# Performance work log

Measured on AMD Instinct MI355X. Metric: run time of the kernel, lower is better.

## Reference

```python
import jax, jax.numpy as jnp
import numpy as np

N_HEADS = 8
D_K = 64
SCALE = D_K ** -0.5


def setup_inputs() -> dict:
    key = jax.random.key(0)
    ks = jax.random.split(key, 5)
    B, C, H, W = 4, 512, 32, 32
    x = jax.random.normal(ks[0], (B, C, H, W), dtype=jnp.float32)
    Wp = jax.random.normal(ks[1], (3 * N_HEADS * D_K, C), dtype=jnp.float32) * (C ** -0.5)
    bp = jax.random.normal(ks[2], (3 * N_HEADS * D_K,), dtype=jnp.float32) * 0.02
    Wo = jax.random.normal(ks[3], (C, N_HEADS * D_K), dtype=jnp.float32) * ((N_HEADS * D_K) ** -0.5)
    bo = jax.random.normal(ks[4], (C,), dtype=jnp.float32) * 0.02
    return {"x": x, "Wp": Wp, "bp": bp, "Wo": Wo, "bo": bo}


def reference(x, Wp, bp, Wo, bo):
    # x: [B, C, H, W]; NOTE: the torch module defines GroupNorm but never calls it.
    B, C, H, W = x.shape
    s = H * W
    xs = x.reshape(B, C, s).transpose(0, 2, 1)          # [B, s, C]
    qkv = (xs @ Wp.T + bp).reshape(B, s, N_HEADS, 3 * D_K)
    q, k, v = jnp.split(qkv, 3, axis=-1)                 # each [B, s, h, d]
    attn = jnp.einsum('bihd,bjhd->bijh', q, k) * SCALE   # [B, s, s, h]
    attn = jax.nn.softmax(attn, axis=2)                  # softmax over j (keys)
    res = jnp.einsum('bijh,bjhd->bihd', attn, v)         # [B, s, h, d]
    res = res.reshape(B, s, N_HEADS * D_K)
    out = res @ Wo.T + bo + xs                           # residual add
    return out.transpose(0, 2, 1).reshape(B, C, H, W)
```

## Files before the change

### kernel.cpp

```cpp
#include <hip/hip_runtime.h>
#include <hip/hip_bf16.h>

typedef unsigned short u16;
typedef __attribute__((ext_vector_type(8))) short frag_ab;
typedef __attribute__((ext_vector_type(4))) float f32x4;
typedef _Float16 f16;
typedef __attribute__((ext_vector_type(4))) _Float16 f16x4;

#define LOG2E 1.44269504088896f

__device__ __forceinline__ float fast_exp2(float x) {
    return __builtin_amdgcn_exp2f(x);
}

__device__ __forceinline__ void gload_lds16(const u16* g, u16* s) {
    __builtin_amdgcn_global_load_lds((const __attribute__((address_space(1))) void*)g,
                                     (__attribute__((address_space(3))) void*)s, 16, 0, 0);
}
__device__ __forceinline__ void gload_lds16h(const f16* g, f16* s) {
    __builtin_amdgcn_global_load_lds((const __attribute__((address_space(1))) void*)g,
                                     (__attribute__((address_space(3))) void*)s, 16, 0, 0);
}

__device__ __forceinline__ void gemm64x128_bt_mainloop(
    const u16* __restrict__ A, const u16* __restrict__ B,
    int m0, int n0, f32x4 acc[2][4], u16* lds)
{
    const int tid = threadIdx.x;
    const int lane = tid & 63, quad = lane >> 4, l16 = lane & 15;
    const int wr = ((tid >> 7) & 1) * 32;
    const int wc = ((tid >> 6) & 1) * 64;
    const int srow = tid >> 3;
    const int scol = (tid & 7) * 8;

    u16* Asb[2] = {lds, lds + 12288};
    u16* Bsb[2] = {lds + 4096, lds + 16384};

#define STAGE_128(bi, k0) do {                                                \
        u16* As_ = Asb[bi]; u16* Bs_ = Bsb[bi];                               \
        _Pragma("unroll")                                                     \
        for (int p = 0; p < 2; ++p) {                                         \
            const int r = srow + p * 32;                                      \
            gload_lds16(A + (size_t)(m0 + r) * 512 + (k0) + scol,             \
                        As_ + r * 64 + scol);                                 \
        }                                                                     \
        _Pragma("unroll")                                                     \
        for (int p = 0; p < 4; ++p) {                                         \
            const int r = srow + p * 32;                                      \
            gload_lds16(B + (size_t)(n0 + r) * 512 + (k0) + scol,             \
                        Bs_ + r * 64 + scol);                                 \
        }                                                                     \
    } while (0)

    STAGE_128(0, 0);
    __syncthreads();
    #pragma unroll
    for (int t = 0; t < 8; ++t) {
        const int cur = t & 1;
        if (t < 7) STAGE_128(cur ^ 1, (t + 1) * 64);
        u16* Asc = Asb[cur];
        u16* Bsc = Bsb[cur];
        #pragma unroll
        for (int ks = 0; ks < 2; ++ks) {
            frag_ab a[2], b[4];
            #pragma unroll
            for (int mt = 0; mt < 2; ++mt)
                a[mt] = *(const frag_ab*)(Asc + (wr + mt * 16 + l16) * 64 + ks * 32 + quad * 8);
            #pragma unroll
            for (int nt = 0; nt < 4; ++nt)
                b[nt] = *(const frag_ab*)(Bsc + (wc + nt * 16 + l16) * 64 + ks * 32 + quad * 8);
            #pragma unroll
            for (int mt = 0; mt < 2; ++mt)
                #pragma unroll
                for (int nt = 0; nt < 4; ++nt)
                    acc[mt][nt] = __builtin_amdgcn_mfma_f32_16x16x32_bf16(a[mt], b[nt], acc[mt][nt], 0, 0, 0);
        }
        if (t < 7) __syncthreads();
    }
#undef STAGE_128
}

__device__ __forceinline__ void gemm64x64_bt_mainloop(
    const u16* __restrict__ A, const u16* __restrict__ B,
    int m0, int n0, f32x4 acc[2][2], u16* lds)
{
    const int tid = threadIdx.x;
    const int lane = tid & 63, quad = lane >> 4, l16 = lane & 15;
    const int wr = ((tid >> 7) & 1) * 32;
    const int wc = ((tid >> 6) & 1) * 32;
    const int srow = tid >> 3;
    const int scol = (tid & 7) * 8;

    u16* Asb[2] = {lds, lds + 8192};
    u16* Bsb[2] = {lds + 4096, lds + 12288};

#define STAGE_64(bi, k0) do {                                                 \
        u16* As_ = Asb[bi]; u16* Bs_ = Bsb[bi];                               \
        _Pragma("unroll")                                                     \
        for (int p = 0; p < 2; ++p) {                                         \
            const int r = srow + p * 32;                                      \
            gload_lds16(A + (size_t)(m0 + r) * 512 + (k0) + scol,             \
                        As_ + r * 64 + scol);                                 \
            gload_lds16(B + (size_t)(n0 + r) * 512 + (k0) + scol,             \
                        Bs_ + r * 64 + scol);                                 \
        }                                                                     \
    } while (0)

    STAGE_64(0, 0);
    __syncthreads();
    #pragma unroll
    for (int t = 0; t < 8; ++t) {
        const int cur = t & 1;
        if (t < 7) STAGE_64(cur ^ 1, (t + 1) * 64);
        u16* Asc = Asb[cur];
        u16* Bsc = Bsb[cur];
        #pragma unroll
        for (int ks = 0; ks < 2; ++ks) {
            frag_ab a[2], b[2];
            #pragma unroll
            for (int mt = 0; mt < 2; ++mt)
                a[mt] = *(const frag_ab*)(Asc + (wr + mt * 16 + l16) * 64 + ks * 32 + quad * 8);
            #pragma unroll
            for (int nt = 0; nt < 2; ++nt)
                b[nt] = *(const frag_ab*)(Bsc + (wc + nt * 16 + l16) * 64 + ks * 32 + quad * 8);
            #pragma unroll
            for (int mt = 0; mt < 2; ++mt)
                #pragma unroll
                for (int nt = 0; nt < 2; ++nt)
                    acc[mt][nt] = __builtin_amdgcn_mfma_f32_16x16x32_bf16(a[mt], b[nt], acc[mt][nt], 0, 0, 0);
        }
        if (t < 7) __syncthreads();
    }
#undef STAGE_64
}

__global__ __launch_bounds__(256) void prep_kernel(
    const float* __restrict__ x, __hip_bfloat16* __restrict__ xs_bf,
    const float* __restrict__ Wp, const float* __restrict__ Wo,
    __hip_bfloat16* __restrict__ w_bf)
{
    __shared__ float tile[32][33];
    const int tid = threadIdx.x;
    const int id = blockIdx.x;
    if (id < 2048) {
        const int i0 = (id & 31) * 32;
        const int c0 = ((id >> 5) & 15) * 32;
        const int b  = id >> 9;
        const int tx = tid & 31, ty = tid >> 5;
        const float* xp = x + ((size_t)b * 512 + c0) * 1024 + i0;
        #pragma unroll
        for (int r = ty; r < 32; r += 8)
            tile[r][tx] = xp[(size_t)r * 1024 + tx];
        __syncthreads();
        __hip_bfloat16* op = xs_bf + ((size_t)b * 1024 + i0) * 512 + c0;
        #pragma unroll
        for (int r = ty; r < 32; r += 8)
            op[(size_t)r * 512 + tx] = __float2bfloat16(tile[tx][r]);
    } else {
        const int t = (id - 2048) * 256 + tid;
        const int i4 = t * 4;
        const float* src = (i4 < 786432) ? (Wp + i4) : (Wo + (i4 - 786432));
        const float4 v = *(const float4*)src;
        ushort4 o;
        o.x = __bfloat16_as_ushort(__float2bfloat16(v.x));
        o.y = __bfloat16_as_ushort(__float2bfloat16(v.y));
        o.z = __bfloat16_as_ushort(__float2bfloat16(v.z));
        o.w = __bfloat16_as_ushort(__float2bfloat16(v.w));
        *(ushort4*)((u16*)w_bf + i4) = o;
    }
}

__global__ __launch_bounds__(256) void qkv_gemm_kernel(
    const u16* __restrict__ Wpb, const u16* __restrict__ xsb,
    const float* __restrict__ bp,
    u16* __restrict__ Qb, u16* __restrict__ Kb, f16* __restrict__ VtT)
{
    __shared__ u16 lds[24576];
    f32x4 acc[2][4];
    #pragma unroll
    for (int mt = 0; mt < 2; ++mt)
        #pragma unroll
        for (int nt = 0; nt < 4; ++nt)
            { acc[mt][nt][0]=0.f; acc[mt][nt][1]=0.f; acc[mt][nt][2]=0.f; acc[mt][nt][3]=0.f; }
    const int m0 = blockIdx.y * 64;
    const int n0 = blockIdx.x * 128;
    gemm64x128_bt_mainloop(Wpb, xsb, m0, n0, acc, lds);

    const int tid = threadIdx.x;
    const int lane = tid & 63, quad = lane >> 4, l16 = lane & 15;
    const int wr = ((tid >> 7) & 1) * 32, wc = ((tid >> 6) & 1) * 64;
    const int h = blockIdx.y / 3, part = blockIdx.y % 3;
    const int b = blockIdx.x >> 3, ipb = (blockIdx.x & 7) * 128;
    const size_t bh = (size_t)(b * 8 + h);

    if (part < 2) {
        const float scale = (part == 0) ? (0.125f * LOG2E) : 1.0f;
        __syncthreads();
        u16* T = lds;
        #pragma unroll
        for (int nt = 0; nt < 4; ++nt) {
            const int px = wc + nt * 16 + l16;
            #pragma unroll
            for (int mt = 0; mt < 2; ++mt) {
                const int cb = m0 + wr + mt * 16 + quad * 4;
                ushort4 pk;
                pk.x = __bfloat16_as_ushort(__float2bfloat16((acc[mt][nt][0] + bp[cb + 0]) * scale));
                pk.y = __bfloat16_as_ushort(__float2bfloat16((acc[mt][nt][1] + bp[cb + 1]) * scale));
                pk.z = __bfloat16_as_ushort(__float2bfloat16((acc[mt][nt][2] + bp[cb + 2]) * scale));
                pk.w = __bfloat16_as_ushort(__float2bfloat16((acc[mt][nt][3] + bp[cb + 3]) * scale));
                *(ushort4*)&T[px * 72 + wr + mt * 16 + quad * 4] = pk;
            }
        }
        __syncthreads();
        u16* dst = (part == 0 ? Qb : Kb);
        #pragma unroll
        for (int p = 0; p < 4; ++p) {
            const int row = p * 32 + (tid >> 3);
            const int ch8 = (tid & 7) * 8;
            uint4 rv = *(uint4*)&T[row * 72 + ch8];
            *(uint4*)(dst + ((bh * 1024 + ipb + row) << 6) + ch8) = rv;
        }
    } else {
        f16* dst = VtT + bh * 65536;
        #pragma unroll
        for (int mt = 0; mt < 2; ++mt) {
            #pragma unroll
            for (int r = 0; r < 4; ++r) {
                const int d = wr + mt * 16 + quad * 4 + r;
                const float bias = bp[m0 + d];
                #pragma unroll
                for (int nt = 0; nt < 4; ++nt) {
                    const int j = ipb + wc + nt * 16 + l16;
                    dst[(size_t)(j >> 3) * 512 + d * 8 + (j & 7)] =
                        (f16)(acc[mt][nt][r] + bias);
                }
            }
        }
    }
}

__global__ __launch_bounds__(256, 2) void attn_kernel(
    const u16* __restrict__ Qb, const u16* __restrict__ Kb,
    const f16* __restrict__ VtT, __hip_bfloat16* __restrict__ resb)
{
    __shared__ float Opart[4][32][68];
    __shared__ float Lpart[4][4][16];
    const int bh = blockIdx.x;
    const int it = blockIdx.y;
    const int tid = threadIdx.x;
    const int w = tid >> 6, lane = tid & 63, quad = lane >> 4, l16 = lane & 15;

    const u16* Qp = Qb + (size_t)bh * 65536;
    const u16* Kp = Kb + (size_t)bh * 65536;
    const f16* Vp = VtT + (size_t)bh * 65536;

    frag_ab bq[4][2];
    #pragma unroll
    for (int ig = 0; ig < 4; ++ig) {
        const u16* qptr = Qp + (size_t)(it * 64 + ig * 16 + l16) * 64 + quad * 8;
        bq[ig][0] = *(const frag_ab*)(qptr);
        bq[ig][1] = *(const frag_ab*)(qptr + 32);
    }

    f32x4 o[4][4];
    #pragma unroll
    for (int ig = 0; ig < 4; ++ig)
        #pragma unroll
        for (int dt = 0; dt < 4; ++dt)
            { o[ig][dt][0]=0.f; o[ig][dt][1]=0.f; o[ig][dt][2]=0.f; o[ig][dt][3]=0.f; }
    float l_acc[4] = {0.f, 0.f, 0.f, 0.f};

    const u16* kbase = Kp + (size_t)(w * 32 + l16) * 64 + quad * 8;
    const f16* vbase = Vp + (size_t)(w * 4 + (quad >> 1)) * 512 + l16 * 8 + (quad & 1) * 4;

#define LOADKV(JT, KA, VA) do {                                              \
        const u16* kp_ = kbase + (size_t)(JT) * 8192;                        \
        KA[0][0] = *(const frag_ab*)(kp_);                                   \
        KA[0][1] = *(const frag_ab*)(kp_ + 32);                              \
        KA[1][0] = *(const frag_ab*)(kp_ + 1024);                            \
        KA[1][1] = *(const frag_ab*)(kp_ + 1056);                            \
        const f16* vp_ = vbase + (size_t)(JT) * 8192;                        \
        _Pragma("unroll")                                                    \
        for (int dt_ = 0; dt_ < 4; ++dt_) {                                  \
            VA[dt_][0] = *(const f16x4*)(vp_ + dt_ * 128);                   \
            VA[dt_][1] = *(const f16x4*)(vp_ + 1024 + dt_ * 128);            \
        }                                                                    \
    } while (0)

#define COMPUTE(KA, VA) do {                                                 \
        _Pragma("unroll")                                                    \
        for (int ig = 0; ig < 4; ++ig) {                                     \
            f32x4 st0 = {0.f, 0.f, 0.f, 0.f}, st1 = {0.f, 0.f, 0.f, 0.f};    \
            st0 = __builtin_amdgcn_mfma_f32_16x16x32_bf16(KA[0][0], bq[ig][0], st0, 0, 0, 0); \
            st0 = __builtin_amdgcn_mfma_f32_16x16x32_bf16(KA[0][1], bq[ig][1], st0, 0, 0, 0); \
            st1 = __builtin_amdgcn_mfma_f32_16x16x32_bf16(KA[1][0], bq[ig][0], st1, 0, 0, 0); \
            st1 = __builtin_amdgcn_mfma_f32_16x16x32_bf16(KA[1][1], bq[ig][1], st1, 0, 0, 0); \
            f16x4 p0, p1;                                                    \
            float s = 0.f;                                                   \
            _Pragma("unroll")                                                \
            for (int r = 0; r < 4; ++r) {                                    \
                const float e0 = fast_exp2(st0[r]);                          \
                const float e1 = fast_exp2(st1[r]);                          \
                s += e0 + e1;                                                \
                p0[r] = (f16)e0;                                             \
                p1[r] = (f16)e1;                                             \
            }                                                                \
            l_acc[ig] += s;                                                  \
            _Pragma("unroll")                                                \
            for (int dt = 0; dt < 4; ++dt) {                                 \
                o[ig][dt] = __builtin_amdgcn_mfma_f32_16x16x16f16(VA[dt][0], p0, o[ig][dt], 0, 0, 0); \
                o[ig][dt] = __builtin_amdgcn_mfma_f32_16x16x16f16(VA[dt][1], p1, o[ig][dt], 0, 0, 0); \
            }                                                                \
        }                                                                    \
    } while (0)

    frag_ab ka0[2][2], ka1[2][2];
    f16x4 va0[4][2], va1[4][2];
    LOADKV(0, ka0, va0);
    #pragma unroll
    for (int jt = 0; jt < 8; jt += 2) {
        LOADKV(jt + 1, ka1, va1);
        COMPUTE(ka0, va0);
        if (jt < 6)
            LOADKV(jt + 2, ka0, va0);
        COMPUTE(ka1, va1);
    }
#undef LOADKV
#undef COMPUTE

    #pragma unroll
    for (int ig = 0; ig < 4; ++ig) {
        l_acc[ig] += __shfl_xor(l_acc[ig], 16);
        l_acc[ig] += __shfl_xor(l_acc[ig], 32);
    }
    if (lane < 16) {
        #pragma unroll
        for (int ig = 0; ig < 4; ++ig)
            Lpart[w][ig][lane] = l_acc[ig];
    }

    const int bb = bh >> 3, hh = bh & 7;
    const int il = tid >> 3, d0 = (tid & 7) * 8;
    #pragma unroll
    for (int ph = 0; ph < 2; ++ph) {
        __syncthreads();
        #pragma unroll
        for (int g = 0; g < 2; ++g) {
            const int ig = ph * 2 + g;
            #pragma unroll
            for (int dt = 0; dt < 4; ++dt)
                *(f32x4*)&Opart[w][g * 16 + l16][dt * 16 + quad * 4] = o[ig][dt];
        }
        __syncthreads();
        f32x4 sa = *(const f32x4*)&Opart[0][il][d0];
        f32x4 sb = *(const f32x4*)&Opart[0][il][d0 + 4];
        #pragma unroll
        for (int ww = 1; ww < 4; ++ww) {
            sa += *(const f32x4*)&Opart[ww][il][d0];
            sb += *(const f32x4*)&Opart[ww][il][d0 + 4];
        }
        const int ig = ph * 2 + (il >> 4);
        const float linv = 1.f / (Lpart[0][ig][il & 15] + Lpart[1][ig][il & 15] +
                                  Lpart[2][ig][il & 15] + Lpart[3][ig][il & 15]);
        u16 pk[8];
        #pragma unroll
        for (int e = 0; e < 4; ++e) {
            pk[e]     = __bfloat16_as_ushort(__float2bfloat16(sa[e] * linv));
            pk[e + 4] = __bfloat16_as_ushort(__float2bfloat16(sb[e] * linv));
        }
        u16* orow = (u16*)resb +
            ((size_t)(bb * 1024 + it * 64 + ph * 32 + il)) * 512 + hh * 64 + d0;
        *(uint4*)orow = *(uint4*)pk;
    }
}

__global__ __launch_bounds__(256) void out_gemm_kernel(
    const u16* __restrict__ Wob, const u16* __restrict__ resb,
    const float* __restrict__ bo, const float* __restrict__ x,
    float* __restrict__ out)
{
    __shared__ u16 lds[16384];
    f32x4 acc[2][2];
    #pragma unroll
    for (int mt = 0; mt < 2; ++mt)
        #pragma unroll
        for (int nt = 0; nt < 2; ++nt)
            { acc[mt][nt][0]=0.f; acc[mt][nt][1]=0.f; acc[mt][nt][2]=0.f; acc[mt][nt][3]=0.f; }
    const int m0 = blockIdx.x * 64;
    const int n0 = blockIdx.y * 64;
    gemm64x64_bt_mainloop(Wob, resb, m0, n0, acc, lds);

    const int tid = threadIdx.x;
    const int lane = tid & 63, quad = lane >> 4, l16 = lane & 15;
    const int wr = ((tid >> 7) & 1) * 32, wc = ((tid >> 6) & 1) * 32;
    #pragma unroll
    for (int nt = 0; nt < 2; ++nt) {
        const int pix = n0 + wc + nt * 16 + l16;
        const int b = pix >> 10, ip = pix & 1023;
        #pragma unroll
        for (int mt = 0; mt < 2; ++mt) {
            #pragma unroll
            for (int r = 0; r < 4; ++r) {
                const int c = m0 + wr + mt * 16 + quad * 4 + r;
                const size_t oidx = (((size_t)b * 512 + c) << 10) + ip;
                out[oidx] = acc[mt][nt][r] + bo[c] + x[oidx];
            }
        }
    }
}

extern "C" void kernel_launch(void* const* d_in, const int* in_sizes, int n_in,
                              void* d_out, int out_size, void* d_ws, size_t ws_size,
                              hipStream_t stream)
{
    const float* x  = (const float*)d_in[0];
    const float* Wp = (const float*)d_in[1];
    const float* bp = (const float*)d_in[2];
    const float* Wo = (const float*)d_in[3];
    const float* bo = (const float*)d_in[4];
    float* out = (float*)d_out;

    char* ws = (char*)d_ws;
    size_t off = 0;
    auto carve = [&](size_t bytes) -> void* {
        void* ptr = ws + off;
        off += (bytes + 255) & ~(size_t)255;
        return ptr;
    };
    __hip_bfloat16* xs_bf = (__hip_bfloat16*)carve((size_t)4096 * 512 * 2);
    __hip_bfloat16* Wp_bf = (__hip_bfloat16*)carve((size_t)1536 * 512 * 2);
    __hip_bfloat16* Wo_bf = (__hip_bfloat16*)carve((size_t)512 * 512 * 2);
    u16*            Qb    = (u16*)carve((size_t)32 * 1024 * 64 * 2);
    u16*            Kb    = (u16*)carve((size_t)32 * 1024 * 64 * 2);
    f16*            VtT   = (f16*)carve((size_t)32 * 1024 * 64 * 2);
    __hip_bfloat16* resb  = (__hip_bfloat16*)carve((size_t)4096 * 512 * 2);

    prep_kernel<<<dim3(3072), 256, 0, stream>>>(x, xs_bf, Wp, Wo, Wp_bf);
    qkv_gemm_kernel<<<dim3(32, 24), 256, 0, stream>>>(
        (const u16*)Wp_bf, (const u16*)xs_bf, bp, Qb, Kb, VtT);
    attn_kernel<<<dim3(32, 16), 256, 0, stream>>>(Qb, Kb, VtT, resb);
    out_gemm_kernel<<<dim3(8, 64), 256, 0, stream>>>(
        (const u16*)Wo_bf, (const u16*)resb, bo, x, out);
    (void)Wo_bf; (void)ws_size; (void)in_sizes; (void)n_in; (void)out_size;
}
```

Measured before the change: 111.0 us.

## Fuse all stages into one persistent cooperative kernel with grid syncs

After: 313.6 us. +182.6%, slower.

```diff
diff --git a/kernel.cpp b/kernel.cpp
--- a/kernel.cpp
+++ b/kernel.cpp
@@ -1,5 +1,8 @@
 #include <hip/hip_runtime.h>
 #include <hip/hip_bf16.h>
+#include <hip/hip_cooperative_groups.h>
+
+namespace cg = cooperative_groups;
 
 typedef unsigned short u16;
 typedef __attribute__((ext_vector_type(8))) short frag_ab;
@@ -14,10 +17,6 @@
 }
 
 __device__ __forceinline__ void gload_lds16(const u16* g, u16* s) {
-    __builtin_amdgcn_global_load_lds((const __attribute__((address_space(1))) void*)g,
-                                     (__attribute__((address_space(3))) void*)s, 16, 0, 0);
-}
-__device__ __forceinline__ void gload_lds16h(const f16* g, f16* s) {
     __builtin_amdgcn_global_load_lds((const __attribute__((address_space(1))) void*)g,
                                      (__attribute__((address_space(3))) void*)s, 16, 0, 0);
 }
@@ -134,15 +133,13 @@
 #undef STAGE_64
 }
 
-__global__ __launch_bounds__(256) void prep_kernel(
-    const float* __restrict__ x, __hip_bfloat16* __restrict__ xs_bf,
+__device__ __forceinline__ void prep_task(
+    int id, int tid, const float* __restrict__ x, __hip_bfloat16* __restrict__ xs_bf,
     const float* __restrict__ Wp, const float* __restrict__ Wo,
-    __hip_bfloat16* __restrict__ w_bf)
-{
-    __shared__ float tile[32][33];
-    const int tid = threadIdx.x;
-    const int id = blockIdx.x;
+    __hip_bfloat16* __restrict__ w_bf, u16* lds_raw)
+{
     if (id < 2048) {
+        float (*tile)[33] = (float(*)[33])lds_raw;
         const int i0 = (id & 31) * 32;
         const int c0 = ((id >> 5) & 15) * 32;
         const int b  = id >> 9;
@@ -170,27 +167,28 @@
     }
 }
 
-__global__ __launch_bounds__(256) void qkv_gemm_kernel(
-    const u16* __restrict__ Wpb, const u16* __restrict__ xsb,
+__device__ __forceinline__ void qkv_task(
+    int t, const u16* __restrict__ Wpb, const u16* __restrict__ xsb,
     const float* __restrict__ bp,
-    u16* __restrict__ Qb, u16* __restrict__ Kb, f16* __restrict__ VtT)
-{
-    __shared__ u16 lds[24576];
+    u16* __restrict__ Qb, u16* __restrict__ Kb, f16* __restrict__ VtT,
+    u16* lds)
+{
     f32x4 acc[2][4];
     #pragma unroll
     for (int mt = 0; mt < 2; ++mt)
         #pragma unroll
         for (int nt = 0; nt < 4; ++nt)
             { acc[mt][nt][0]=0.f; acc[mt][nt][1]=0.f; acc[mt][nt][2]=0.f; acc[mt][nt][3]=0.f; }
-    const int m0 = blockIdx.y * 64;
-    const int n0 = blockIdx.x * 128;
+    const int ty = t >> 5, tx = t & 31;
+    const int m0 = ty * 64;
+    const int n0 = tx * 128;
     gemm64x128_bt_mainloop(Wpb, xsb, m0, n0, acc, lds);
 
     const int tid = threadIdx.x;
     const int lane = tid & 63, quad = lane >> 4, l16 = lane & 15;
     const int wr = ((tid >> 7) & 1) * 32, wc = ((tid >> 6) & 1) * 64;
-    const int h = blockIdx.y / 3, part = blockIdx.y % 3;
-    const int b = blockIdx.x >> 3, ipb = (blockIdx.x & 7) * 128;
+    const int h = ty / 3, part = ty % 3;
+    const int b = tx >> 3, ipb = (tx & 7) * 128;
     const size_t bh = (size_t)(b * 8 + h);
 
     if (part < 2) {
@@ -239,14 +237,13 @@
     }
 }
 
-__global__ __launch_bounds__(256, 2) void attn_kernel(
-    const u16* __restrict__ Qb, const u16* __restrict__ Kb,
-    const f16* __restrict__ VtT, __hip_bfloat16* __restrict__ resb)
-{
-    __shared__ float Opart[4][32][68];
-    __shared__ float Lpart[4][4][16];
-    const int bh = blockIdx.x;
-    const int it = blockIdx.y;
+__device__ __forceinline__ void attn_task(
+    int bh, int it, const u16* __restrict__ Qb, const u16* __restrict__ Kb,
+    const f16* __restrict__ VtT, __hip_bfloat16* __restrict__ resb,
+    u16* lds_raw)
+{
+    float (*Opart)[32][68] = (float(*)[32][68])lds_raw;
+    float (*Lpart)[4][16]  = (float(*)[4][16])((char*)lds_raw + 34816);
     const int tid = threadIdx.x;
     const int w = tid >> 6, lane = tid & 63, quad = lane >> 4, l16 = lane & 15;
 
@@ -374,20 +371,17 @@
     }
 }
 
-__global__ __launch_bounds__(256) void out_gemm_kernel(
-    const u16* __restrict__ Wob, const u16* __restrict__ resb,
+__device__ __forceinline__ void out_task(
+    int m0, int n0, const u16* __restrict__ Wob, const u16* __restrict__ resb,
     const float* __restrict__ bo, const float* __restrict__ x,
-    float* __restrict__ out)
-{
-    __shared__ u16 lds[16384];
+    float* __restrict__ out, u16* lds)
+{
     f32x4 acc[2][2];
     #pragma unroll
     for (int mt = 0; mt < 2; ++mt)
         #pragma unroll
         for (int nt = 0; nt < 2; ++nt)
             { acc[mt][nt][0]=0.f; acc[mt][nt][1]=0.f; acc[mt][nt][2]=0.f; acc[mt][nt][3]=0.f; }
-    const int m0 = blockIdx.x * 64;
-    const int n0 = blockIdx.y * 64;
     gemm64x64_bt_mainloop(Wob, resb, m0, n0, acc, lds);
 
     const int tid = threadIdx.x;
@@ -407,6 +401,87 @@
             }
         }
     }
+}
+
+__global__ __launch_bounds__(256, 2) void fused_kernel(
+    const float* __restrict__ x, const float* __restrict__ Wp,
+    const float* __restrict__ bp, const float* __restrict__ Wo,
+    const float* __restrict__ bo, float* __restrict__ out,
+    __hip_bfloat16* __restrict__ xs_bf, __hip_bfloat16* __restrict__ w_bf,
+    u16* __restrict__ Qb, u16* __restrict__ Kb, f16* __restrict__ VtT,
+    __hip_bfloat16* __restrict__ resb, int* __restrict__ qkv_ctr)
+{
+    __shared__ __align__(16) u16 lds_raw[24576];
+    __shared__ int s_task;
+    cg::grid_group grid = cg::this_grid();
+    const int blk = blockIdx.x;
+    const int tid = threadIdx.x;
+
+    if (blk == 0 && tid == 0) *qkv_ctr = 0;
+    #pragma unroll 1
+    for (int kk = 0; kk < 6; ++kk) {
+        prep_task(blk + kk * 512, tid, x, xs_bf, Wp, Wo, w_bf, lds_raw);
+        __syncthreads();
+    }
+    grid.sync();
+
+    {
+        const u16* Wpb = (const u16*)w_bf;
+        const u16* xsb = (const u16*)xs_bf;
+        for (;;) {
+            if (tid == 0) s_task = atomicAdd(qkv_ctr, 1);
+            __syncthreads();
+            const int t = s_task;
+            if (t >= 768) break;
+            qkv_task(t, Wpb, xsb, bp, Qb, Kb, VtT, lds_raw);
+            __syncthreads();
+        }
+    }
+    grid.sync();
+
+    attn_task(blk & 31, blk >> 5, Qb, Kb, VtT, resb, lds_raw);
+    grid.sync();
+
+    {
+        const u16* Wob = (const u16*)(w_bf + (size_t)1536 * 512);
+        out_task((blk & 7) * 64, (blk >> 3) * 64, Wob, (const u16*)resb,
+                 bo, x, out, lds_raw);
+    }
+}
+
+__global__ __launch_bounds__(256) void prep_kernel(
+    const float* __restrict__ x, __hip_bfloat16* __restrict__ xs_bf,
+    const float* __restrict__ Wp, const float* __restrict__ Wo,
+    __hip_bfloat16* __restrict__ w_bf)
+{
+    __shared__ __align__(16) u16 lds_raw[2112];
+    prep_task(blockIdx.x, threadIdx.x, x, xs_bf, Wp, Wo, w_bf, lds_raw);
+}
+
+__global__ __launch_bounds__(256) void qkv_gemm_kernel(
+    const u16* __restrict__ Wpb, const u16* __restrict__ xsb,
+    const float* __restrict__ bp,
+    u16* __restrict__ Qb, u16* __restrict__ Kb, f16* __restrict__ VtT)
+{
+    __shared__ __align__(16) u16 lds_raw[24576];
+    qkv_task(blockIdx.y * 32 + blockIdx.x, Wpb, xsb, bp, Qb, Kb, VtT, lds_raw);
+}
+
+__global__ __launch_bounds__(256, 2) void attn_kernel(
+    const u16* __restrict__ Qb, const u16* __restrict__ Kb,
+    const f16* __restrict__ VtT, __hip_bfloat16* __restrict__ resb)
+{
+    __shared__ __align__(16) u16 lds_raw[17920];
+    attn_task(blockIdx.x, blockIdx.y, Qb, Kb, VtT, resb, lds_raw);
+}
+
+__global__ __launch_bounds__(256) void out_gemm_kernel(
+    const u16* __restrict__ Wob, const u16* __restrict__ resb,
+    const float* __restrict__ bo, const float* __restrict__ x,
+    float* __restrict__ out)
+{
+    __shared__ __align__(16) u16 lds_raw[16384];
+    out_task(blockIdx.x * 64, blockIdx.y * 64, Wob, resb, bo, x, out, lds_raw);
 }
 
 extern "C" void kernel_launch(void* const* d_in, const int* in_sizes, int n_in,
@@ -434,12 +509,23 @@
     u16*            Kb    = (u16*)carve((size_t)32 * 1024 * 64 * 2);
     f16*            VtT   = (f16*)carve((size_t)32 * 1024 * 64 * 2);
     __hip_bfloat16* resb  = (__hip_bfloat16*)carve((size_t)4096 * 512 * 2);
-
-    prep_kernel<<<dim3(3072), 256, 0, stream>>>(x, xs_bf, Wp, Wo, Wp_bf);
-    qkv_gemm_kernel<<<dim3(32, 24), 256, 0, stream>>>(
-        (const u16*)Wp_bf, (const u16*)xs_bf, bp, Qb, Kb, VtT);
-    attn_kernel<<<dim3(32, 16), 256, 0, stream>>>(Qb, Kb, VtT, resb);
-    out_gemm_kernel<<<dim3(8, 64), 256, 0, stream>>>(
-        (const u16*)Wo_bf, (const u16*)resb, bo, x, out);
+    int*            qctr  = (int*)carve(256);
+
+    void* args[] = {
+        (void*)&x, (void*)&Wp, (void*)&bp, (void*)&Wo, (void*)&bo, (void*)&out,
+        (void*)&xs_bf, (void*)&Wp_bf, (void*)&Qb, (void*)&Kb, (void*)&VtT,
+        (void*)&resb, (void*)&qctr
+    };
+    hipError_t e = hipLaunchCooperativeKernel((const void*)fused_kernel,
+                                              dim3(512), dim3(256), args, 0, stream);
+    if (e != hipSuccess) {
+        (void)hipGetLastError();
+        prep_kernel<<<dim3(3072), 256, 0, stream>>>(x, xs_bf, Wp, Wo, Wp_bf);
+        qkv_gemm_kernel<<<dim3(32, 24), 256, 0, stream>>>(
+            (const u16*)Wp_bf, (const u16*)xs_bf, bp, Qb, Kb, VtT);
+        attn_kernel<<<dim3(32, 16), 256, 0, stream>>>(Qb, Kb, VtT, resb);
+        out_gemm_kernel<<<dim3(8, 64), 256, 0, stream>>>(
+            (const u16*)Wo_bf, (const u16*)resb, bo, x, out);
+    }
     (void)Wo_bf; (void)ws_size; (void)in_sizes; (void)n_in; (void)out_size;
 }
```

## Split attention key range across 8 waves with 512-thread blocks and setprio

Applied to the files above, without the earlier changes.

Result: slower. 141.9 us (+27.9%).

```diff
diff --git a/kernel.cpp b/kernel.cpp
--- a/kernel.cpp
+++ b/kernel.cpp
@@ -14,10 +14,6 @@
 }
 
 __device__ __forceinline__ void gload_lds16(const u16* g, u16* s) {
-    __builtin_amdgcn_global_load_lds((const __attribute__((address_space(1))) void*)g,
-                                     (__attribute__((address_space(3))) void*)s, 16, 0, 0);
-}
-__device__ __forceinline__ void gload_lds16h(const f16* g, f16* s) {
     __builtin_amdgcn_global_load_lds((const __attribute__((address_space(1))) void*)g,
                                      (__attribute__((address_space(3))) void*)s, 16, 0, 0);
 }
@@ -239,12 +235,12 @@
     }
 }
 
-__global__ __launch_bounds__(256, 2) void attn_kernel(
+__global__ __launch_bounds__(512, 4) void attn_kernel(
     const u16* __restrict__ Qb, const u16* __restrict__ Kb,
     const f16* __restrict__ VtT, __hip_bfloat16* __restrict__ resb)
 {
-    __shared__ float Opart[4][32][68];
-    __shared__ float Lpart[4][4][16];
+    __shared__ float Opart[4][64][68];
+    __shared__ float Lpart[8][4][16];
     const int bh = blockIdx.x;
     const int it = blockIdx.y;
     const int tid = threadIdx.x;
@@ -270,63 +266,47 @@
             { o[ig][dt][0]=0.f; o[ig][dt][1]=0.f; o[ig][dt][2]=0.f; o[ig][dt][3]=0.f; }
     float l_acc[4] = {0.f, 0.f, 0.f, 0.f};
 
-    const u16* kbase = Kp + (size_t)(w * 32 + l16) * 64 + quad * 8;
-    const f16* vbase = Vp + (size_t)(w * 4 + (quad >> 1)) * 512 + l16 * 8 + (quad & 1) * 4;
-
-#define LOADKV(JT, KA, VA) do {                                              \
-        const u16* kp_ = kbase + (size_t)(JT) * 8192;                        \
-        KA[0][0] = *(const frag_ab*)(kp_);                                   \
-        KA[0][1] = *(const frag_ab*)(kp_ + 32);                              \
-        KA[1][0] = *(const frag_ab*)(kp_ + 1024);                            \
-        KA[1][1] = *(const frag_ab*)(kp_ + 1056);                            \
-        const f16* vp_ = vbase + (size_t)(JT) * 8192;                        \
-        _Pragma("unroll")                                                    \
-        for (int dt_ = 0; dt_ < 4; ++dt_) {                                  \
-            VA[dt_][0] = *(const f16x4*)(vp_ + dt_ * 128);                   \
-            VA[dt_][1] = *(const f16x4*)(vp_ + 1024 + dt_ * 128);            \
-        }                                                                    \
-    } while (0)
-
-#define COMPUTE(KA, VA) do {                                                 \
-        _Pragma("unroll")                                                    \
-        for (int ig = 0; ig < 4; ++ig) {                                     \
-            f32x4 st0 = {0.f, 0.f, 0.f, 0.f}, st1 = {0.f, 0.f, 0.f, 0.f};    \
-            st0 = __builtin_amdgcn_mfma_f32_16x16x32_bf16(KA[0][0], bq[ig][0], st0, 0, 0, 0); \
-            st0 = __builtin_amdgcn_mfma_f32_16x16x32_bf16(KA[0][1], bq[ig][1], st0, 0, 0, 0); \
-            st1 = __builtin_amdgcn_mfma_f32_16x16x32_bf16(KA[1][0], bq[ig][0], st1, 0, 0, 0); \
-            st1 = __builtin_amdgcn_mfma_f32_16x16x32_bf16(KA[1][1], bq[ig][1], st1, 0, 0, 0); \
-            f16x4 p0, p1;                                                    \
-            float s = 0.f;                                                   \
-            _Pragma("unroll")                                                \
-            for (int r = 0; r < 4; ++r) {                                    \
-                const float e0 = fast_exp2(st0[r]);                          \
-                const float e1 = fast_exp2(st1[r]);                          \
-                s += e0 + e1;                                                \
-                p0[r] = (f16)e0;                                             \
-                p1[r] = (f16)e1;                                             \
-            }                                                                \
-            l_acc[ig] += s;                                                  \
-            _Pragma("unroll")                                                \
-            for (int dt = 0; dt < 4; ++dt) {                                 \
-                o[ig][dt] = __builtin_amdgcn_mfma_f32_16x16x16f16(VA[dt][0], p0, o[ig][dt], 0, 0, 0); \
-                o[ig][dt] = __builtin_amdgcn_mfma_f32_16x16x16f16(VA[dt][1], p1, o[ig][dt], 0, 0, 0); \
-            }                                                                \
-        }                                                                    \
-    } while (0)
-
-    frag_ab ka0[2][2], ka1[2][2];
-    f16x4 va0[4][2], va1[4][2];
-    LOADKV(0, ka0, va0);
-    #pragma unroll
-    for (int jt = 0; jt < 8; jt += 2) {
-        LOADKV(jt + 1, ka1, va1);
-        COMPUTE(ka0, va0);
-        if (jt < 6)
-            LOADKV(jt + 2, ka0, va0);
-        COMPUTE(ka1, va1);
-    }
-#undef LOADKV
-#undef COMPUTE
+    const u16* kbase = Kp + (size_t)(w * 16 + l16) * 64 + quad * 8;
+    const f16* vbase = Vp + (size_t)(w * 2 + (quad >> 1)) * 512 + l16 * 8 + (quad & 1) * 4;
+
+    #pragma unroll
+    for (int jt = 0; jt < 8; ++jt) {
+        frag_ab ka[2];
+        {
+            const u16* kp_ = kbase + (size_t)jt * 8192;
+            ka[0] = *(const frag_ab*)(kp_);
+            ka[1] = *(const frag_ab*)(kp_ + 32);
+        }
+        f16x4 va[4];
+        {
+            const f16* vp_ = vbase + (size_t)jt * 8192;
+            #pragma unroll
+            for (int dt = 0; dt < 4; ++dt)
+                va[dt] = *(const f16x4*)(vp_ + dt * 128);
+        }
+        #pragma unroll
+        for (int ig = 0; ig < 4; ++ig) {
+            f32x4 st = {0.f, 0.f, 0.f, 0.f};
+            __builtin_amdgcn_s_setprio(1);
+            st = __builtin_amdgcn_mfma_f32_16x16x32_bf16(ka[0], bq[ig][0], st, 0, 0, 0);
+            st = __builtin_amdgcn_mfma_f32_16x16x32_bf16(ka[1], bq[ig][1], st, 0, 0, 0);
+            __builtin_amdgcn_s_setprio(0);
+            f16x4 p;
+            float s = 0.f;
+            #pragma unroll
+            for (int r = 0; r < 4; ++r) {
+                const float e = fast_exp2(st[r]);
+                s += e;
+                p[r] = (f16)e;
+            }
+            l_acc[ig] += s;
+            __builtin_amdgcn_s_setprio(1);
+            #pragma unroll
+            for (int dt = 0; dt < 4; ++dt)
+                o[ig][dt] = __builtin_amdgcn_mfma_f32_16x16x16f16(va[dt], p, o[ig][dt], 0, 0, 0);
+            __builtin_amdgcn_s_setprio(0);
+        }
+    }
 
     #pragma unroll
     for (int ig = 0; ig < 4; ++ig) {
@@ -341,37 +321,53 @@
 
     const int bb = bh >> 3, hh = bh & 7;
     const int il = tid >> 3, d0 = (tid & 7) * 8;
-    #pragma unroll
-    for (int ph = 0; ph < 2; ++ph) {
-        __syncthreads();
-        #pragma unroll
-        for (int g = 0; g < 2; ++g) {
-            const int ig = ph * 2 + g;
+
+    __syncthreads();
+    if (w < 4) {
+        #pragma unroll
+        for (int ig = 0; ig < 4; ++ig)
             #pragma unroll
             for (int dt = 0; dt < 4; ++dt)
-                *(f32x4*)&Opart[w][g * 16 + l16][dt * 16 + quad * 4] = o[ig][dt];
-        }
-        __syncthreads();
-        f32x4 sa = *(const f32x4*)&Opart[0][il][d0];
-        f32x4 sb = *(const f32x4*)&Opart[0][il][d0 + 4];
-        #pragma unroll
-        for (int ww = 1; ww < 4; ++ww) {
-            sa += *(const f32x4*)&Opart[ww][il][d0];
-            sb += *(const f32x4*)&Opart[ww][il][d0 + 4];
-        }
-        const int ig = ph * 2 + (il >> 4);
-        const float linv = 1.f / (Lpart[0][ig][il & 15] + Lpart[1][ig][il & 15] +
-                                  Lpart[2][ig][il & 15] + Lpart[3][ig][il & 15]);
-        u16 pk[8];
-        #pragma unroll
-        for (int e = 0; e < 4; ++e) {
-            pk[e]     = __bfloat16_as_ushort(__float2bfloat16(sa[e] * linv));
-            pk[e + 4] = __bfloat16_as_ushort(__float2bfloat16(sb[e] * linv));
-        }
-        u16* orow = (u16*)resb +
-            ((size_t)(bb * 1024 + it * 64 + ph * 32 + il)) * 512 + hh * 64 + d0;
-        *(uint4*)orow = *(uint4*)pk;
-    }
+                *(f32x4*)&Opart[w][ig * 16 + l16][dt * 16 + quad * 4] = o[ig][dt];
+    }
+    __syncthreads();
+    f32x4 sa = *(const f32x4*)&Opart[0][il][d0];
+    f32x4 sb = *(const f32x4*)&Opart[0][il][d0 + 4];
+    #pragma unroll
+    for (int ww = 1; ww < 4; ++ww) {
+        sa += *(const f32x4*)&Opart[ww][il][d0];
+        sb += *(const f32x4*)&Opart[ww][il][d0 + 4];
+    }
+    __syncthreads();
+    if (w >= 4) {
+        #pragma unroll
+        for (int ig = 0; ig < 4; ++ig)
+            #pragma unroll
+            for (int dt = 0; dt < 4; ++dt)
+                *(f32x4*)&Opart[w - 4][ig * 16 + l16][dt * 16 + quad * 4] = o[ig][dt];
+    }
+    __syncthreads();
+    #pragma unroll
+    for (int ww = 0; ww < 4; ++ww) {
+        sa += *(const f32x4*)&Opart[ww][il][d0];
+        sb += *(const f32x4*)&Opart[ww][il][d0 + 4];
+    }
+
+    const int ig = il >> 4;
+    float lsum = 0.f;
+    #pragma unroll
+    for (int ww = 0; ww < 8; ++ww)
+        lsum += Lpart[ww][ig][il & 15];
+    const float linv = 1.f / lsum;
+    u16 pk[8];
+    #pragma unroll
+    for (int e = 0; e < 4; ++e) {
+        pk[e]     = __bfloat16_as_ushort(__float2bfloat16(sa[e] * linv));
+        pk[e + 4] = __bfloat16_as_ushort(__float2bfloat16(sb[e] * linv));
+    }
+    u16* orow = (u16*)resb +
+        ((size_t)(bb * 1024 + it * 64 + il)) * 512 + hh * 64 + d0;
+    *(uint4*)orow = *(uint4*)pk;
 }
 
 __global__ __launch_bounds__(256) void out_gemm_kernel(
@@ -438,7 +434,7 @@
     prep_kernel<<<dim3(3072), 256, 0, stream>>>(x, xs_bf, Wp, Wo, Wp_bf);
     qkv_gemm_kernel<<<dim3(32, 24), 256, 0, stream>>>(
         (const u16*)Wp_bf, (const u16*)xs_bf, bp, Qb, Kb, VtT);
-    attn_kernel<<<dim3(32, 16), 256, 0, stream>>>(Qb, Kb, VtT, resb);
+    attn_kernel<<<dim3(32, 16), 512, 0, stream>>>(Qb, Kb, VtT, resb);
     out_gemm_kernel<<<dim3(8, 64), 256, 0, stream>>>(
         (const u16*)Wo_bf, (const u16*)resb, bo, x, out);
     (void)Wo_bf; (void)ws_size; (void)in_sizes; (void)n_in; (void)out_size;
```
